# Optimization experiments

Hardware: AMD Instinct MI355X
Metric: run time of the kernel (lower is better)

## Reference

```python
import jax, jax.numpy as jnp
import numpy as np

N = 100000   # nodes
E = 1600000  # edges
IN = 64      # in_channels
H = 128      # hidden_features
G = 1024     # graphs in batch
NUM_REST = 3 # num_layers (extra GraphConv layers)


def setup_inputs() -> dict:
    key = jax.random.key(0)
    ks = jax.random.split(key, 12)
    x = jax.random.normal(ks[0], (N, IN), jnp.float32)
    edge_index = jax.random.randint(ks[1], (2, E), 0, N)
    edge_attr = jax.random.uniform(ks[2], (E,), jnp.float32)
    batch = jnp.sort(jax.random.randint(ks[3], (N,), 0, G))

    def glorot(k, shape, fan_in):
        return jax.random.normal(k, shape, jnp.float32) / np.float32(np.sqrt(fan_in))

    # GraphConv layer 0: in -> hidden (lin_root: no bias, lin_rel: bias)
    W_root0 = glorot(ks[4], (H, IN), IN)
    W_rel0 = glorot(ks[5], (H, IN), IN)
    b0 = jnp.zeros((H,), jnp.float32)
    # GraphConv layers 1..3: hidden -> hidden (stacked)
    W_root_r = glorot(ks[6], (NUM_REST, H, H), H)
    W_rel_r = glorot(ks[7], (NUM_REST, H, H), H)
    b_r = jnp.zeros((NUM_REST, H), jnp.float32)
    # MLPReadout: [H -> H//2 -> 1]
    Wr1 = glorot(ks[8], (H // 2, H), H)
    br1 = jnp.zeros((H // 2,), jnp.float32)
    Wr2 = glorot(ks[9], (1, H // 2), H // 2)
    br2 = jnp.zeros((1,), jnp.float32)
    return dict(x=x, edge_index=edge_index, edge_attr=edge_attr, batch=batch,
                W_root0=W_root0, W_rel0=W_rel0, b0=b0,
                W_root_r=W_root_r, W_rel_r=W_rel_r, b_r=b_r,
                Wr1=Wr1, br1=br1, Wr2=Wr2, br2=br2)


def graph_conv(x, src, dst, ew, W_root, W_rel, b):
    # PyG GraphConv (aggr='add'):
    #   out_i = W_rel @ sum_{j->i} e_ji * x_j + b + W_root @ x_i
    msg = ew[:, None] * x[src]                                   # [E, d]
    agg = jax.ops.segment_sum(msg, dst, num_segments=x.shape[0])  # [N, d]
    return agg @ W_rel.T + b + x @ W_root.T


def reference(x, edge_index, edge_attr, batch,
              W_root0, W_rel0, b0, W_root_r, W_rel_r, b_r,
              Wr1, br1, Wr2, br2):
    src, dst = edge_index[0], edge_index[1]
    y = graph_conv(x, src, dst, edge_attr, W_root0, W_rel0, b0)
    for l in range(W_root_r.shape[0]):
        y = graph_conv(y, src, dst, edge_attr, W_root_r[l], W_rel_r[l], b_r[l])
    # MLPReadout: Linear -> ReLU -> Linear
    y = jax.nn.relu(y @ Wr1.T + br1)
    y = y @ Wr2.T + br2                                           # [N, 1]
    # scatter-mean over graph assignment
    num = jax.ops.segment_sum(y, batch, num_segments=G)           # [G, 1]
    cnt = jax.ops.segment_sum(jnp.ones((y.shape[0], 1), y.dtype), batch,
                              num_segments=G)
    return num / jnp.maximum(cnt, 1.0)                            # [G, 1]
```

## Files before the change

### kernel.cpp

```cpp
#include <hip/hip_runtime.h>
#include <hip/hip_fp16.h>
#include <cstdint>
#include <cstddef>

#define NNODES 100000
#define NEDGES 1600000
#define NGRAPH 1024
#define NB_SCAN ((NNODES + 255) / 256)
#define FILL_CHUNK 4096
#define FILL_NCHUNK ((NEDGES + FILL_CHUNK - 1) / FILL_CHUNK)
#define SHARD 12500

typedef __attribute__((ext_vector_type(8))) short short8;
typedef __attribute__((ext_vector_type(8))) unsigned short ushort8;
typedef __attribute__((ext_vector_type(4))) float f32x4;

__device__ inline float b2f(unsigned short u) {
  return __uint_as_float(((unsigned int)u) << 16);
}
__device__ inline unsigned short f2b(float f) {
  unsigned int x = __float_as_uint(f);
  x += 0x7fffu + ((x >> 16) & 1u);
  return (unsigned short)(x >> 16);
}
__device__ inline unsigned int pack_edge(int src, float w) {
  unsigned short hb = __half_as_ushort(__float2half_rn(w));
  return ((unsigned int)src << 15) | ((unsigned int)hb >> 1);
}
__device__ inline void unpack_edge(unsigned int p, int& src, float& w) {
  src = (int)(p >> 15);
  w = __half2float(__ushort_as_half((unsigned short)((p & 0x7fffu) << 1)));
}

__global__ __launch_bounds__(256) void prepack_kernel(
    const float* __restrict__ Wrel0, const float* __restrict__ Wroot0,
    const float* __restrict__ WrelR, const float* __restrict__ WrootR,
    const float* __restrict__ Wr1, unsigned short* __restrict__ dst)
{
  int g = blockIdx.x * 256 + threadIdx.x;
  if (g >= 15360) return;
  const float* src; int H, K, r; unsigned short* out;
  if (g < 1024)       { src = Wrel0;  H = 128; K = 64;  r = g;        out = dst + r * 8; }
  else if (g < 2048)  { src = Wroot0; H = 128; K = 64;  r = g - 1024; out = dst + 8192 + r * 8; }
  else if (g < 8192)  { int m = g - 2048; int l = m / 2048; r = m % 2048;
                        src = WrelR + l * 16384;  H = 128; K = 128;
                        out = dst + 16384 + l * 16384 + r * 8; }
  else if (g < 14336) { int m = g - 8192; int l = m / 2048; r = m % 2048;
                        src = WrootR + l * 16384; H = 128; K = 128;
                        out = dst + 65536 + l * 16384 + r * 8; }
  else                { src = Wr1;    H = 64;  K = 128; r = g - 14336; out = dst + 114688 + r * 8; }
  int n = r % H, k8 = r / H;
  const float* s = src + (size_t)n * K + k8 * 8;
#pragma unroll
  for (int j = 0; j < 8; j++) out[j] = f2b(s[j]);
}

__global__ __launch_bounds__(256) void cvt_x_kernel(
    const float* __restrict__ x, unsigned short* __restrict__ xb)
{
  int i = blockIdx.x * 256 + threadIdx.x;
  if (i * 4 >= NNODES * 64) return;
  float4 v = *(const float4*)(x + i * 4);
  ushort4 o;
  o.x = f2b(v.x); o.y = f2b(v.y); o.z = f2b(v.z); o.w = f2b(v.w);
  *(ushort4*)(xb + i * 4) = o;
}

__global__ __launch_bounds__(256) void hist_kernel(
    const int* __restrict__ ei, int* __restrict__ deg)
{
  int e = blockIdx.x * 256 + threadIdx.x;
  if (e < NEDGES) atomicAdd(&deg[ei[NEDGES + e]], 1);
}

__global__ __launch_bounds__(256) void scan1_kernel(
    const int* __restrict__ deg, int* __restrict__ exloc, int* __restrict__ bsum)
{
  __shared__ int s[256];
  int i = blockIdx.x * 256 + threadIdx.x;
  int v = (i < NNODES) ? deg[i] : 0;
  s[threadIdx.x] = v;
  __syncthreads();
#pragma unroll
  for (int off = 1; off < 256; off <<= 1) {
    int t = (threadIdx.x >= off) ? s[threadIdx.x - off] : 0;
    __syncthreads();
    s[threadIdx.x] += t;
    __syncthreads();
  }
  if (i < NNODES) exloc[i] = s[threadIdx.x] - v;
  if (threadIdx.x == 255) bsum[blockIdx.x] = s[255];
}

__global__ __launch_bounds__(512) void scan2_kernel(int* __restrict__ bsum)
{
  __shared__ int s[512];
  int v = (threadIdx.x < NB_SCAN) ? bsum[threadIdx.x] : 0;
  s[threadIdx.x] = v;
  __syncthreads();
#pragma unroll
  for (int off = 1; off < 512; off <<= 1) {
    int t = (threadIdx.x >= off) ? s[threadIdx.x - off] : 0;
    __syncthreads();
    s[threadIdx.x] += t;
    __syncthreads();
  }
  if (threadIdx.x < NB_SCAN) bsum[threadIdx.x] = s[threadIdx.x] - v;
}

__global__ __launch_bounds__(256) void scan3_kernel(
    const int* __restrict__ exloc, const int* __restrict__ bsum,
    int* __restrict__ row_ptr, int* __restrict__ row_fill)
{
  int i = blockIdx.x * 256 + threadIdx.x;
  if (i < NNODES) {
    int v = exloc[i] + bsum[blockIdx.x];
    row_ptr[i] = v;
    row_fill[i] = v;
  }
  if (i == 0) row_ptr[NNODES] = NEDGES;
}

__global__ __launch_bounds__(256) void fill_kernel(
    const int* __restrict__ ei, const float* __restrict__ ew,
    int* __restrict__ row_fill, unsigned int* __restrict__ epack)
{
  int chunk = blockIdx.x >> 3;
  int shard = blockIdx.x & 7;
  int base = chunk * FILL_CHUNK;
  for (int t = threadIdx.x; t < FILL_CHUNK; t += 256) {
    int e = base + t;
    if (e >= NEDGES) break;
    int d = ei[NEDGES + e];
    if ((unsigned)d / SHARD == (unsigned)shard) {
      int p = atomicAdd(&row_fill[d], 1);
      epack[p] = pack_edge(ei[e], ew[e]);
    }
  }
}

__global__ __launch_bounds__(256) void gptr_kernel(
    const int* __restrict__ batch, int* __restrict__ gptr)
{
  int i = blockIdx.x * 256 + threadIdx.x;
  if (i >= NNODES) return;
  int b = batch[i];
  int bn = (i + 1 < NNODES) ? batch[i + 1] : NGRAPH;
  for (int g = b + 1; g <= bn; g++) gptr[g] = i + 1;
  if (i == 0) for (int g = 0; g <= b; g++) gptr[g] = 0;
}

__global__ __launch_bounds__(256) void agg128_kernel(
    const int* __restrict__ row_ptr, const unsigned int* __restrict__ epack,
    const unsigned short* __restrict__ x, unsigned short* __restrict__ agg)
{
  int node = blockIdx.x * 4 + (threadIdx.x >> 6);
  int lane = threadIdx.x & 63;
  if (node >= NNODES) return;
  int q = lane >> 4, sl = lane & 15;
  int s = row_ptr[node], e = row_ptr[node + 1];
  float acc[8];
#pragma unroll
  for (int j = 0; j < 8; j++) acc[j] = 0.f;

  for (int i = s + q; i < e; i += 16) {
    unsigned int p0 = epack[i];
    unsigned int p1 = (i + 4  < e) ? epack[i + 4]  : 0u;
    unsigned int p2 = (i + 8  < e) ? epack[i + 8]  : 0u;
    unsigned int p3 = (i + 12 < e) ? epack[i + 12] : 0u;
    int s0, s1, s2, s3; float w0, w1, w2, w3;
    unpack_edge(p0, s0, w0);
    unpack_edge(p1, s1, w1);
    unpack_edge(p2, s2, w2);
    unpack_edge(p3, s3, w3);
    ushort8 r0 = *(const ushort8*)(x + (size_t)s0 * 128 + sl * 8);
    ushort8 r1 = *(const ushort8*)(x + (size_t)s1 * 128 + sl * 8);
    ushort8 r2 = *(const ushort8*)(x + (size_t)s2 * 128 + sl * 8);
    ushort8 r3 = *(const ushort8*)(x + (size_t)s3 * 128 + sl * 8);
#pragma unroll
    for (int j = 0; j < 8; j++)
      acc[j] += w0 * b2f(r0[j]) + w1 * b2f(r1[j]) +
                w2 * b2f(r2[j]) + w3 * b2f(r3[j]);
  }
#pragma unroll
  for (int j = 0; j < 8; j++) {
    acc[j] += __shfl_xor(acc[j], 16, 64);
    acc[j] += __shfl_xor(acc[j], 32, 64);
  }
  if (q == 0) {
    ushort8 o;
#pragma unroll
    for (int j = 0; j < 8; j++) o[j] = f2b(acc[j]);
    *(ushort8*)(agg + (size_t)node * 128 + sl * 8) = o;
  }
}

__global__ __launch_bounds__(256) void agg64_kernel(
    const int* __restrict__ row_ptr, const unsigned int* __restrict__ epack,
    const unsigned short* __restrict__ x, unsigned short* __restrict__ agg)
{
  int node = blockIdx.x * 4 + (threadIdx.x >> 6);
  int lane = threadIdx.x & 63;
  if (node >= NNODES) return;
  int q = lane >> 3, sl = lane & 7;
  int s = row_ptr[node], e = row_ptr[node + 1];
  float acc[8];
#pragma unroll
  for (int j = 0; j < 8; j++) acc[j] = 0.f;

  for (int i = s + q; i < e; i += 16) {
    unsigned int p0 = epack[i];
    unsigned int p1 = (i + 8 < e) ? epack[i + 8] : 0u;
    int s0, s1; float w0, w1;
    unpack_edge(p0, s0, w0);
    unpack_edge(p1, s1, w1);
    ushort8 r0 = *(const ushort8*)(x + (size_t)s0 * 64 + sl * 8);
    ushort8 r1 = *(const ushort8*)(x + (size_t)s1 * 64 + sl * 8);
#pragma unroll
    for (int j = 0; j < 8; j++)
      acc[j] += w0 * b2f(r0[j]) + w1 * b2f(r1[j]);
  }
#pragma unroll
  for (int j = 0; j < 8; j++) {
    acc[j] += __shfl_xor(acc[j], 8, 64);
    acc[j] += __shfl_xor(acc[j], 16, 64);
    acc[j] += __shfl_xor(acc[j], 32, 64);
  }
  if (q == 0) {
    ushort8 o;
#pragma unroll
    for (int j = 0; j < 8; j++) o[j] = f2b(acc[j]);
    *(ushort8*)(agg + (size_t)node * 64 + sl * 8) = o;
  }
}

template <int KDIM, int HOUT, int MT, bool DUAL, bool RELU>
__global__ __launch_bounds__(256) void mfma_gemm(
    const unsigned short* __restrict__ A1, const unsigned short* __restrict__ W1,
    const unsigned short* __restrict__ A2, const unsigned short* __restrict__ W2,
    const float* __restrict__ bias, unsigned short* __restrict__ out)
{
  constexpr int NT2 = HOUT / 16;
  constexpr int KC = KDIM / 32;
  const int wave = threadIdx.x >> 6, lane = threadIdx.x & 63;
  const int quad = lane >> 4, l16 = lane & 15;
  const int n0 = (blockIdx.x * 4 + wave) * (MT * 16);

  f32x4 acc[MT][NT2];
#pragma unroll
  for (int m = 0; m < MT; m++)
#pragma unroll
    for (int t = 0; t < NT2; t++) acc[m][t] = (f32x4){0.f, 0.f, 0.f, 0.f};

  int nodes[MT];
#pragma unroll
  for (int m = 0; m < MT; m++) {
    int nd = n0 + m * 16 + l16;
    nodes[m] = nd < NNODES ? nd : NNODES - 1;
  }

#pragma unroll
  for (int c = 0; c < KC; c++) {
    short8 bfr[NT2];
#pragma unroll
    for (int t = 0; t < NT2; t++)
      bfr[t] = *(const short8*)(W1 + ((size_t)(c * 4 + quad) * HOUT + t * 16 + l16) * 8);
#pragma unroll
    for (int m = 0; m < MT; m++) {
      short8 af = *(const short8*)(A1 + (size_t)nodes[m] * KDIM + c * 32 + quad * 8);
#pragma unroll
      for (int t = 0; t < NT2; t++)
        acc[m][t] = __builtin_amdgcn_mfma_f32_16x16x32_bf16(af, bfr[t], acc[m][t], 0, 0, 0);
    }
    if (DUAL) {
#pragma unroll
      for (int t = 0; t < NT2; t++)
        bfr[t] = *(const short8*)(W2 + ((size_t)(c * 4 + quad) * HOUT + t * 16 + l16) * 8);
#pragma unroll
      for (int m = 0; m < MT; m++) {
        short8 af = *(const short8*)(A2 + (size_t)nodes[m] * KDIM + c * 32 + quad * 8);
#pragma unroll
        for (int t = 0; t < NT2; t++)
          acc[m][t] = __builtin_amdgcn_mfma_f32_16x16x32_bf16(af, bfr[t], acc[m][t], 0, 0, 0);
      }
    }
  }

#pragma unroll
  for (int m = 0; m < MT; m++) {
    int rowbase = n0 + m * 16 + quad * 4;
#pragma unroll
    for (int t = 0; t < NT2; t++) {
      float b = bias[t * 16 + l16];
#pragma unroll
      for (int r = 0; r < 4; r++) {
        int nd = rowbase + r;
        if (nd < NNODES) {
          float v = acc[m][t][r] + b;
          if (RELU) v = fmaxf(v, 0.f);
          out[(size_t)nd * HOUT + t * 16 + l16] = f2b(v);
        }
      }
    }
  }
}

__global__ __launch_bounds__(256) void readout_reduce_kernel(
    const unsigned short* __restrict__ h, const float* __restrict__ Wr2,
    const float* __restrict__ br2, const int* __restrict__ gptr,
    float* __restrict__ out)
{
  __shared__ float wsum[4];
  int g = blockIdx.x;
  int s = gptr[g], e = gptr[g + 1];
  int wave = threadIdx.x >> 6, lane = threadIdx.x & 63;
  float w2 = Wr2[lane];
  float acc = 0.f;
  for (int n = s + wave; n < e; n += 4)
    acc += b2f(h[(size_t)n * 64 + lane]) * w2;
#pragma unroll
  for (int off = 32; off >= 1; off >>= 1) acc += __shfl_xor(acc, off, 64);
  if (lane == 0) wsum[wave] = acc;
  __syncthreads();
  if (threadIdx.x == 0) {
    float cnt = (float)(e - s);
    float sum = wsum[0] + wsum[1] + wsum[2] + wsum[3] + cnt * br2[0];
    out[g] = sum / fmaxf(cnt, 1.f);
  }
}

extern "C" void kernel_launch(void* const* d_in, const int* in_sizes, int n_in,
                              void* d_out, int out_size, void* d_ws, size_t ws_size,
                              hipStream_t stream)
{
  const float* x      = (const float*)d_in[0];
  const int*   ei     = (const int*)d_in[1];
  const float* ew     = (const float*)d_in[2];
  const int*   batch  = (const int*)d_in[3];
  const float* Wroot0 = (const float*)d_in[4];
  const float* Wrel0  = (const float*)d_in[5];
  const float* b0     = (const float*)d_in[6];
  const float* WrootR = (const float*)d_in[7];
  const float* WrelR  = (const float*)d_in[8];
  const float* bR     = (const float*)d_in[9];
  const float* Wr1    = (const float*)d_in[10];
  const float* br1    = (const float*)d_in[11];
  const float* Wr2    = (const float*)d_in[12];
  const float* br2    = (const float*)d_in[13];

  char* ws = (char*)d_ws;
  unsigned short* wp   = (unsigned short*)ws;
  unsigned short* xb   = wp + 131072;
  unsigned short* agg0 = xb + (size_t)NNODES * 64;
  unsigned short* bufA = agg0 + (size_t)NNODES * 64;
  unsigned short* bufB = bufA + (size_t)NNODES * 128;
  unsigned short* hbuf = bufB + (size_t)NNODES * 128;
  int*  deg      = (int*)(hbuf + (size_t)NNODES * 64);
  int*  exloc    = deg + NNODES;
  int*  row_ptr  = exloc + NNODES;
  int*  row_fill = row_ptr + NNODES + 2;
  int*  bsum     = row_fill + NNODES;
  int*  gptr     = bsum + 512;
  unsigned int* epack = (unsigned int*)(gptr + NGRAPH + 2);

  prepack_kernel<<<60, 256, 0, stream>>>(Wrel0, Wroot0, WrelR, WrootR, Wr1, wp);
  cvt_x_kernel<<<(NNODES * 64 / 4 + 255) / 256, 256, 0, stream>>>(x, xb);

  const unsigned short* pWrel0  = wp;
  const unsigned short* pWroot0 = wp + 8192;
  const unsigned short* pWrelR  = wp + 16384;
  const unsigned short* pWrootR = wp + 65536;
  const unsigned short* pWr1    = wp + 114688;

  hipMemsetAsync(deg, 0, NNODES * sizeof(int), stream);
  hist_kernel<<<(NEDGES + 255) / 256, 256, 0, stream>>>(ei, deg);
  scan1_kernel<<<NB_SCAN, 256, 0, stream>>>(deg, exloc, bsum);
  scan2_kernel<<<1, 512, 0, stream>>>(bsum);
  scan3_kernel<<<NB_SCAN, 256, 0, stream>>>(exloc, bsum, row_ptr, row_fill);
  fill_kernel<<<FILL_NCHUNK * 8, 256, 0, stream>>>(ei, ew, row_fill, epack);
  gptr_kernel<<<(NNODES + 255) / 256, 256, 0, stream>>>(batch, gptr);

  agg64_kernel<<<(NNODES + 3) / 4, 256, 0, stream>>>(row_ptr, epack, xb, agg0);
  mfma_gemm<64, 128, 2, true, false><<<(NNODES + 127) / 128, 256, 0, stream>>>(
      agg0, pWrel0, xb, pWroot0, b0, bufB);

  unsigned short* bufs[2] = { bufB, bufA };
  for (int l = 0; l < 3; l++) {
    unsigned short* in  = bufs[l & 1];
    unsigned short* agg = bufs[(l & 1) ^ 1];
    agg128_kernel<<<(NNODES + 3) / 4, 256, 0, stream>>>(row_ptr, epack, in, agg);
    mfma_gemm<128, 128, 2, true, false><<<(NNODES + 127) / 128, 256, 0, stream>>>(
        agg, pWrelR + l * 16384, in, pWrootR + l * 16384, bR + l * 128, agg);
  }

  mfma_gemm<128, 64, 4, false, true><<<(NNODES + 255) / 256, 256, 0, stream>>>(
      bufA, pWr1, nullptr, nullptr, br1, hbuf);
  readout_reduce_kernel<<<NGRAPH, 256, 0, stream>>>(hbuf, Wr2, br2, gptr, (float*)d_out);
}
```

Before: 593.3 us.

## Fuse neighbor aggregation and dual GEMM into one per-layer kernel via LDS

Each GraphConv layer now runs as a single kernel: a block gathers and aggregates 128 nodes into a padded shared-memory tile, then runs the rel and root MFMA GEMMs directly from LDS and the input features. This removes the global write and read of the aggregated tensor and one launch per layer. The trade-off is lower parallelism in the aggregation phase (one block per 128 nodes, each wave walking 32 nodes in sequence) and load imbalance across nodes with uneven degree. Edge-index loads in the CSR build are also switched to nontemporal loads.

```diff
diff --git a/kernel.cpp b/kernel.cpp
--- a/kernel.cpp
+++ b/kernel.cpp
@@ -70,7 +70,7 @@
     const int* __restrict__ ei, int* __restrict__ deg)
 {
   int e = blockIdx.x * 256 + threadIdx.x;
-  if (e < NEDGES) atomicAdd(&deg[ei[NEDGES + e]], 1);
+  if (e < NEDGES) atomicAdd(&deg[__builtin_nontemporal_load(ei + NEDGES + e)], 1);
 }
 
 __global__ __launch_bounds__(256) void scan1_kernel(
@@ -131,10 +131,12 @@
   for (int t = threadIdx.x; t < FILL_CHUNK; t += 256) {
     int e = base + t;
     if (e >= NEDGES) break;
-    int d = ei[NEDGES + e];
+    int d = __builtin_nontemporal_load(ei + NEDGES + e);
     if ((unsigned)d / SHARD == (unsigned)shard) {
+      int src = __builtin_nontemporal_load(ei + e);
+      float w = __builtin_nontemporal_load(ew + e);
       int p = atomicAdd(&row_fill[d], 1);
-      epack[p] = pack_edge(ei[e], ew[e]);
+      epack[p] = pack_edge(src, w);
     }
   }
 }
@@ -150,94 +152,156 @@
   if (i == 0) for (int g = 0; g <= b; g++) gptr[g] = 0;
 }
 
-__global__ __launch_bounds__(256) void agg128_kernel(
+template <int KDIM, int ROWP>
+__global__ __launch_bounds__(256) void fused_layer_kernel(
     const int* __restrict__ row_ptr, const unsigned int* __restrict__ epack,
-    const unsigned short* __restrict__ x, unsigned short* __restrict__ agg)
-{
-  int node = blockIdx.x * 4 + (threadIdx.x >> 6);
-  int lane = threadIdx.x & 63;
-  if (node >= NNODES) return;
-  int q = lane >> 4, sl = lane & 15;
-  int s = row_ptr[node], e = row_ptr[node + 1];
-  float acc[8];
-#pragma unroll
-  for (int j = 0; j < 8; j++) acc[j] = 0.f;
-
-  for (int i = s + q; i < e; i += 16) {
-    unsigned int p0 = epack[i];
-    unsigned int p1 = (i + 4  < e) ? epack[i + 4]  : 0u;
-    unsigned int p2 = (i + 8  < e) ? epack[i + 8]  : 0u;
-    unsigned int p3 = (i + 12 < e) ? epack[i + 12] : 0u;
-    int s0, s1, s2, s3; float w0, w1, w2, w3;
-    unpack_edge(p0, s0, w0);
-    unpack_edge(p1, s1, w1);
-    unpack_edge(p2, s2, w2);
-    unpack_edge(p3, s3, w3);
-    ushort8 r0 = *(const ushort8*)(x + (size_t)s0 * 128 + sl * 8);
-    ushort8 r1 = *(const ushort8*)(x + (size_t)s1 * 128 + sl * 8);
-    ushort8 r2 = *(const ushort8*)(x + (size_t)s2 * 128 + sl * 8);
-    ushort8 r3 = *(const ushort8*)(x + (size_t)s3 * 128 + sl * 8);
-#pragma unroll
-    for (int j = 0; j < 8; j++)
-      acc[j] += w0 * b2f(r0[j]) + w1 * b2f(r1[j]) +
-                w2 * b2f(r2[j]) + w3 * b2f(r3[j]);
-  }
-#pragma unroll
-  for (int j = 0; j < 8; j++) {
-    acc[j] += __shfl_xor(acc[j], 16, 64);
-    acc[j] += __shfl_xor(acc[j], 32, 64);
-  }
-  if (q == 0) {
-    ushort8 o;
-#pragma unroll
-    for (int j = 0; j < 8; j++) o[j] = f2b(acc[j]);
-    *(ushort8*)(agg + (size_t)node * 128 + sl * 8) = o;
-  }
-}
-
-__global__ __launch_bounds__(256) void agg64_kernel(
-    const int* __restrict__ row_ptr, const unsigned int* __restrict__ epack,
-    const unsigned short* __restrict__ x, unsigned short* __restrict__ agg)
-{
-  int node = blockIdx.x * 4 + (threadIdx.x >> 6);
-  int lane = threadIdx.x & 63;
-  if (node >= NNODES) return;
-  int q = lane >> 3, sl = lane & 7;
-  int s = row_ptr[node], e = row_ptr[node + 1];
-  float acc[8];
-#pragma unroll
-  for (int j = 0; j < 8; j++) acc[j] = 0.f;
-
-  for (int i = s + q; i < e; i += 16) {
-    unsigned int p0 = epack[i];
-    unsigned int p1 = (i + 8 < e) ? epack[i + 8] : 0u;
-    int s0, s1; float w0, w1;
-    unpack_edge(p0, s0, w0);
-    unpack_edge(p1, s1, w1);
-    ushort8 r0 = *(const ushort8*)(x + (size_t)s0 * 64 + sl * 8);
-    ushort8 r1 = *(const ushort8*)(x + (size_t)s1 * 64 + sl * 8);
-#pragma unroll
-    for (int j = 0; j < 8; j++)
-      acc[j] += w0 * b2f(r0[j]) + w1 * b2f(r1[j]);
-  }
-#pragma unroll
-  for (int j = 0; j < 8; j++) {
-    acc[j] += __shfl_xor(acc[j], 8, 64);
-    acc[j] += __shfl_xor(acc[j], 16, 64);
-    acc[j] += __shfl_xor(acc[j], 32, 64);
-  }
-  if (q == 0) {
-    ushort8 o;
-#pragma unroll
-    for (int j = 0; j < 8; j++) o[j] = f2b(acc[j]);
-    *(ushort8*)(agg + (size_t)node * 64 + sl * 8) = o;
-  }
-}
-
-template <int KDIM, int HOUT, int MT, bool DUAL, bool RELU>
+    const unsigned short* __restrict__ xin,
+    const unsigned short* __restrict__ W_rel, const unsigned short* __restrict__ W_root,
+    const float* __restrict__ bias, unsigned short* __restrict__ out)
+{
+  __shared__ unsigned short sAgg[128 * ROWP];
+  const int wave = threadIdx.x >> 6, lane = threadIdx.x & 63;
+  const int nbase = blockIdx.x * 128;
+
+  if (KDIM == 128) {
+    int q = lane >> 4, sl = lane & 15;
+#pragma unroll 2
+    for (int t = 0; t < 32; t++) {
+      int nl = wave * 32 + t;
+      int node = nbase + nl;
+      int s = 0, e = 0;
+      if (node < NNODES) { s = row_ptr[node]; e = row_ptr[node + 1]; }
+      float acc[8];
+#pragma unroll
+      for (int j = 0; j < 8; j++) acc[j] = 0.f;
+      for (int i = s + q; i < e; i += 16) {
+        unsigned int p0 = epack[i];
+        unsigned int p1 = (i + 4  < e) ? epack[i + 4]  : 0u;
+        unsigned int p2 = (i + 8  < e) ? epack[i + 8]  : 0u;
+        unsigned int p3 = (i + 12 < e) ? epack[i + 12] : 0u;
+        int s0, s1, s2, s3; float w0, w1, w2, w3;
+        unpack_edge(p0, s0, w0); unpack_edge(p1, s1, w1);
+        unpack_edge(p2, s2, w2); unpack_edge(p3, s3, w3);
+        ushort8 r0 = *(const ushort8*)(xin + (size_t)s0 * 128 + sl * 8);
+        ushort8 r1 = *(const ushort8*)(xin + (size_t)s1 * 128 + sl * 8);
+        ushort8 r2 = *(const ushort8*)(xin + (size_t)s2 * 128 + sl * 8);
+        ushort8 r3 = *(const ushort8*)(xin + (size_t)s3 * 128 + sl * 8);
+#pragma unroll
+        for (int j = 0; j < 8; j++)
+          acc[j] += w0 * b2f(r0[j]) + w1 * b2f(r1[j]) +
+                    w2 * b2f(r2[j]) + w3 * b2f(r3[j]);
+      }
+#pragma unroll
+      for (int j = 0; j < 8; j++) {
+        acc[j] += __shfl_xor(acc[j], 16, 64);
+        acc[j] += __shfl_xor(acc[j], 32, 64);
+      }
+      if (q == 0) {
+        ushort8 o;
+#pragma unroll
+        for (int j = 0; j < 8; j++) o[j] = f2b(acc[j]);
+        *(ushort8*)(sAgg + nl * ROWP + sl * 8) = o;
+      }
+    }
+  } else {
+    int q = lane >> 3, sl = lane & 7;
+#pragma unroll 2
+    for (int t = 0; t < 32; t++) {
+      int nl = wave * 32 + t;
+      int node = nbase + nl;
+      int s = 0, e = 0;
+      if (node < NNODES) { s = row_ptr[node]; e = row_ptr[node + 1]; }
+      float acc[8];
+#pragma unroll
+      for (int j = 0; j < 8; j++) acc[j] = 0.f;
+      for (int i = s + q; i < e; i += 16) {
+        unsigned int p0 = epack[i];
+        unsigned int p1 = (i + 8 < e) ? epack[i + 8] : 0u;
+        int s0, s1; float w0, w1;
+        unpack_edge(p0, s0, w0); unpack_edge(p1, s1, w1);
+        ushort8 r0 = *(const ushort8*)(xin + (size_t)s0 * 64 + sl * 8);
+        ushort8 r1 = *(const ushort8*)(xin + (size_t)s1 * 64 + sl * 8);
+#pragma unroll
+        for (int j = 0; j < 8; j++)
+          acc[j] += w0 * b2f(r0[j]) + w1 * b2f(r1[j]);
+      }
+#pragma unroll
+      for (int j = 0; j < 8; j++) {
+        acc[j] += __shfl_xor(acc[j], 8, 64);
+        acc[j] += __shfl_xor(acc[j], 16, 64);
+        acc[j] += __shfl_xor(acc[j], 32, 64);
+      }
+      if (q == 0) {
+        ushort8 o;
+#pragma unroll
+        for (int j = 0; j < 8; j++) o[j] = f2b(acc[j]);
+        *(ushort8*)(sAgg + nl * ROWP + sl * 8) = o;
+      }
+    }
+  }
+  __syncthreads();
+
+  constexpr int NT2 = 8;
+  constexpr int KC = KDIM / 32;
+  const int quad = lane >> 4, l16 = lane & 15;
+
+  f32x4 acc[2][NT2];
+#pragma unroll
+  for (int m = 0; m < 2; m++)
+#pragma unroll
+    for (int t = 0; t < NT2; t++) acc[m][t] = (f32x4){0.f, 0.f, 0.f, 0.f};
+
+  int nodesg[2];
+#pragma unroll
+  for (int m = 0; m < 2; m++) {
+    int nd = nbase + (wave * 2 + m) * 16 + l16;
+    nodesg[m] = nd < NNODES ? nd : NNODES - 1;
+  }
+
+#pragma unroll
+  for (int c = 0; c < KC; c++) {
+    short8 bfr[NT2];
+#pragma unroll
+    for (int t = 0; t < NT2; t++)
+      bfr[t] = *(const short8*)(W_rel + ((size_t)(c * 4 + quad) * 128 + t * 16 + l16) * 8);
+#pragma unroll
+    for (int m = 0; m < 2; m++) {
+      short8 af = *(const short8*)(sAgg + ((wave * 2 + m) * 16 + l16) * ROWP + c * 32 + quad * 8);
+#pragma unroll
+      for (int t = 0; t < NT2; t++)
+        acc[m][t] = __builtin_amdgcn_mfma_f32_16x16x32_bf16(af, bfr[t], acc[m][t], 0, 0, 0);
+    }
+#pragma unroll
+    for (int t = 0; t < NT2; t++)
+      bfr[t] = *(const short8*)(W_root + ((size_t)(c * 4 + quad) * 128 + t * 16 + l16) * 8);
+#pragma unroll
+    for (int m = 0; m < 2; m++) {
+      short8 af = *(const short8*)(xin + (size_t)nodesg[m] * KDIM + c * 32 + quad * 8);
+#pragma unroll
+      for (int t = 0; t < NT2; t++)
+        acc[m][t] = __builtin_amdgcn_mfma_f32_16x16x32_bf16(af, bfr[t], acc[m][t], 0, 0, 0);
+    }
+  }
+
+#pragma unroll
+  for (int m = 0; m < 2; m++) {
+    int rowbase = nbase + (wave * 2 + m) * 16 + quad * 4;
+#pragma unroll
+    for (int t = 0; t < NT2; t++) {
+      float b = bias[t * 16 + l16];
+#pragma unroll
+      for (int r = 0; r < 4; r++) {
+        int nd = rowbase + r;
+        if (nd < NNODES)
+          out[(size_t)nd * 128 + t * 16 + l16] = f2b(acc[m][t][r] + b);
+      }
+    }
+  }
+}
+
+template <int KDIM, int HOUT, int MT, bool RELU>
 __global__ __launch_bounds__(256) void mfma_gemm(
     const unsigned short* __restrict__ A1, const unsigned short* __restrict__ W1,
-    const unsigned short* __restrict__ A2, const unsigned short* __restrict__ W2,
     const float* __restrict__ bias, unsigned short* __restrict__ out)
 {
   constexpr int NT2 = HOUT / 16;
@@ -271,18 +335,6 @@
 #pragma unroll
       for (int t = 0; t < NT2; t++)
         acc[m][t] = __builtin_amdgcn_mfma_f32_16x16x32_bf16(af, bfr[t], acc[m][t], 0, 0, 0);
-    }
-    if (DUAL) {
-#pragma unroll
-      for (int t = 0; t < NT2; t++)
-        bfr[t] = *(const short8*)(W2 + ((size_t)(c * 4 + quad) * HOUT + t * 16 + l16) * 8);
-#pragma unroll
-      for (int m = 0; m < MT; m++) {
-        short8 af = *(const short8*)(A2 + (size_t)nodes[m] * KDIM + c * 32 + quad * 8);
-#pragma unroll
-        for (int t = 0; t < NT2; t++)
-          acc[m][t] = __builtin_amdgcn_mfma_f32_16x16x32_bf16(af, bfr[t], acc[m][t], 0, 0, 0);
-      }
     }
   }
 
@@ -351,8 +403,7 @@
   char* ws = (char*)d_ws;
   unsigned short* wp   = (unsigned short*)ws;
   unsigned short* xb   = wp + 131072;
-  unsigned short* agg0 = xb + (size_t)NNODES * 64;
-  unsigned short* bufA = agg0 + (size_t)NNODES * 64;
+  unsigned short* bufA = xb + (size_t)NNODES * 64;
   unsigned short* bufB = bufA + (size_t)NNODES * 128;
   unsigned short* hbuf = bufB + (size_t)NNODES * 128;
   int*  deg      = (int*)(hbuf + (size_t)NNODES * 64);
@@ -380,20 +431,20 @@
   fill_kernel<<<FILL_NCHUNK * 8, 256, 0, stream>>>(ei, ew, row_fill, epack);
   gptr_kernel<<<(NNODES + 255) / 256, 256, 0, stream>>>(batch, gptr);
 
-  agg64_kernel<<<(NNODES + 3) / 4, 256, 0, stream>>>(row_ptr, epack, xb, agg0);
-  mfma_gemm<64, 128, 2, true, false><<<(NNODES + 127) / 128, 256, 0, stream>>>(
-      agg0, pWrel0, xb, pWroot0, b0, bufB);
+  const int NLB = (NNODES + 127) / 128;
+
+  fused_layer_kernel<64, 72><<<NLB, 256, 0, stream>>>(
+      row_ptr, epack, xb, pWrel0, pWroot0, b0, bufB);
 
   unsigned short* bufs[2] = { bufB, bufA };
   for (int l = 0; l < 3; l++) {
     unsigned short* in  = bufs[l & 1];
-    unsigned short* agg = bufs[(l & 1) ^ 1];
-    agg128_kernel<<<(NNODES + 3) / 4, 256, 0, stream>>>(row_ptr, epack, in, agg);
-    mfma_gemm<128, 128, 2, true, false><<<(NNODES + 127) / 128, 256, 0, stream>>>(
-        agg, pWrelR + l * 16384, in, pWrootR + l * 16384, bR + l * 128, agg);
-  }
-
-  mfma_gemm<128, 64, 4, false, true><<<(NNODES + 255) / 256, 256, 0, stream>>>(
-      bufA, pWr1, nullptr, nullptr, br1, hbuf);
+    unsigned short* out = bufs[(l & 1) ^ 1];
+    fused_layer_kernel<128, 136><<<NLB, 256, 0, stream>>>(
+        row_ptr, epack, in, pWrelR + l * 16384, pWrootR + l * 16384, bR + l * 128, out);
+  }
+
+  mfma_gemm<128, 64, 4, true><<<(NNODES + 255) / 256, 256, 0, stream>>>(
+      bufA, pWr1, br1, hbuf);
   readout_reduce_kernel<<<NGRAPH, 256, 0, stream>>>(hbuf, Wr2, br2, gptr, (float*)d_out);
 }
```

New measurement: 790.6 us. 33.3% more time.

## Make CSR fill persistent with XCD-affine shard queues; shrink GEMM row tiles

Applied to the files above, without the earlier changes.

The CSR fill kernel becomes a persistent grid of 2048 blocks. Each block reads its XCD id from a hardware register and pulls chunks from per-shard atomic work queues, starting with the shard matching its XCD. The goal is to keep each destination shard's atomics and writes within one XCD's L2 and to balance work dynamically. Separately, the GEMM launches drop the per-block row-tile multiplier to 1 so more, smaller blocks run. This adds a counters buffer and a memset, plus per-chunk block-wide synchronisation and a global atomic.

```diff
diff --git a/kernel.cpp b/kernel.cpp
--- a/kernel.cpp
+++ b/kernel.cpp
@@ -30,6 +30,11 @@
 __device__ inline void unpack_edge(unsigned int p, int& src, float& w) {
   src = (int)(p >> 15);
   w = __half2float(__ushort_as_half((unsigned short)((p & 0x7fffu) << 1)));
+}
+__device__ inline int get_xcd() {
+  unsigned int x;
+  asm volatile("s_getreg_b32 %0, hwreg(HW_REG_XCC_ID)" : "=s"(x));
+  return (int)(x & 7u);
 }
 
 __global__ __launch_bounds__(256) void prepack_kernel(
@@ -60,7 +65,7 @@
 {
   int i = blockIdx.x * 256 + threadIdx.x;
   if (i * 4 >= NNODES * 64) return;
-  float4 v = *(const float4*)(x + i * 4);
+  f32x4 v = *(const f32x4*)(x + i * 4);
   ushort4 o;
   o.x = f2b(v.x); o.y = f2b(v.y); o.z = f2b(v.z); o.w = f2b(v.w);
   *(ushort4*)(xb + i * 4) = o;
@@ -123,18 +128,29 @@
 
 __global__ __launch_bounds__(256) void fill_kernel(
     const int* __restrict__ ei, const float* __restrict__ ew,
-    int* __restrict__ row_fill, unsigned int* __restrict__ epack)
-{
-  int chunk = blockIdx.x >> 3;
-  int shard = blockIdx.x & 7;
-  int base = chunk * FILL_CHUNK;
-  for (int t = threadIdx.x; t < FILL_CHUNK; t += 256) {
-    int e = base + t;
-    if (e >= NEDGES) break;
-    int d = ei[NEDGES + e];
-    if ((unsigned)d / SHARD == (unsigned)shard) {
-      int p = atomicAdd(&row_fill[d], 1);
-      epack[p] = pack_edge(ei[e], ew[e]);
+    int* __restrict__ row_fill, unsigned int* __restrict__ epack,
+    int* __restrict__ counters)
+{
+  __shared__ int sc;
+  int xcd = get_xcd();
+  for (int s2 = 0; s2 < 8; s2++) {
+    int sh = (xcd + s2) & 7;
+    for (;;) {
+      __syncthreads();
+      if (threadIdx.x == 0) sc = atomicAdd(&counters[sh], 1);
+      __syncthreads();
+      int chunk = sc;
+      if (chunk >= FILL_NCHUNK) break;
+      int base = chunk * FILL_CHUNK;
+      for (int t = threadIdx.x; t < FILL_CHUNK; t += 256) {
+        int e = base + t;
+        if (e >= NEDGES) break;
+        int d = ei[NEDGES + e];
+        if ((unsigned)d / SHARD == (unsigned)sh) {
+          int p = atomicAdd(&row_fill[d], 1);
+          epack[p] = pack_edge(ei[e], ew[e]);
+        }
+      }
     }
   }
 }
@@ -361,7 +377,8 @@
   int*  row_fill = row_ptr + NNODES + 2;
   int*  bsum     = row_fill + NNODES;
   int*  gptr     = bsum + 512;
-  unsigned int* epack = (unsigned int*)(gptr + NGRAPH + 2);
+  int*  counters = gptr + NGRAPH + 2;
+  unsigned int* epack = (unsigned int*)(counters + 8);
 
   prepack_kernel<<<60, 256, 0, stream>>>(Wrel0, Wroot0, WrelR, WrootR, Wr1, wp);
   cvt_x_kernel<<<(NNODES * 64 / 4 + 255) / 256, 256, 0, stream>>>(x, xb);
@@ -373,15 +390,16 @@
   const unsigned short* pWr1    = wp + 114688;
 
   hipMemsetAsync(deg, 0, NNODES * sizeof(int), stream);
+  hipMemsetAsync(counters, 0, 8 * sizeof(int), stream);
   hist_kernel<<<(NEDGES + 255) / 256, 256, 0, stream>>>(ei, deg);
   scan1_kernel<<<NB_SCAN, 256, 0, stream>>>(deg, exloc, bsum);
   scan2_kernel<<<1, 512, 0, stream>>>(bsum);
   scan3_kernel<<<NB_SCAN, 256, 0, stream>>>(exloc, bsum, row_ptr, row_fill);
-  fill_kernel<<<FILL_NCHUNK * 8, 256, 0, stream>>>(ei, ew, row_fill, epack);
+  fill_kernel<<<2048, 256, 0, stream>>>(ei, ew, row_fill, epack, counters);
   gptr_kernel<<<(NNODES + 255) / 256, 256, 0, stream>>>(batch, gptr);
 
   agg64_kernel<<<(NNODES + 3) / 4, 256, 0, stream>>>(row_ptr, epack, xb, agg0);
-  mfma_gemm<64, 128, 2, true, false><<<(NNODES + 127) / 128, 256, 0, stream>>>(
+  mfma_gemm<64, 128, 1, true, false><<<(NNODES + 63) / 64, 256, 0, stream>>>(
       agg0, pWrel0, xb, pWroot0, b0, bufB);
 
   unsigned short* bufs[2] = { bufB, bufA };
@@ -389,11 +407,11 @@
     unsigned short* in  = bufs[l & 1];
     unsigned short* agg = bufs[(l & 1) ^ 1];
     agg128_kernel<<<(NNODES + 3) / 4, 256, 0, stream>>>(row_ptr, epack, in, agg);
-    mfma_gemm<128, 128, 2, true, false><<<(NNODES + 127) / 128, 256, 0, stream>>>(
+    mfma_gemm<128, 128, 1, true, false><<<(NNODES + 63) / 64, 256, 0, stream>>>(
         agg, pWrelR + l * 16384, in, pWrootR + l * 16384, bR + l * 128, agg);
   }
 
-  mfma_gemm<128, 64, 4, false, true><<<(NNODES + 255) / 256, 256, 0, stream>>>(
+  mfma_gemm<128, 64, 1, false, true><<<(NNODES + 63) / 64, 256, 0, stream>>>(
       bufA, pWr1, nullptr, nullptr, br1, hbuf);
   readout_reduce_kernel<<<NGRAPH, 256, 0, stream>>>(hbuf, Wr2, br2, gptr, (float*)d_out);
 }
```

After: 792.6 us. 1.34x slower.
